# Performance work log

Measured on AMD Instinct MI355X. Metric: run time of the kernel, lower is better.

The kernel has to match this reference:

```python
import jax, jax.numpy as jnp
import numpy as np

N_EMBD = 1024
N_HEAD = 16
HEAD_DIM = N_EMBD // N_HEAD


def setup_inputs() -> dict:
    key = jax.random.key(0)
    ks = jax.random.split(key, 9)
    B, T, C = 2, 2048, N_EMBD
    s = 1.0 / np.sqrt(C)
    inp = {
        "x": jax.random.normal(ks[0], (B, T, C), dtype=jnp.float32),
        "Wq": jax.random.normal(ks[1], (C, C), dtype=jnp.float32) * s,
        "bq": jnp.zeros((C,), dtype=jnp.float32),
        "Wk": jax.random.normal(ks[2], (C, C), dtype=jnp.float32) * s,
        "bk": jnp.zeros((C,), dtype=jnp.float32),
        "Wv": jax.random.normal(ks[3], (C, C), dtype=jnp.float32) * s,
        "bv": jnp.zeros((C,), dtype=jnp.float32),
        "Wo": jax.random.normal(ks[4], (C, C), dtype=jnp.float32) * s,
        "bo": jnp.zeros((C,), dtype=jnp.float32),
    }
    return inp


def reference(x, Wq, bq, Wk, bk, Wv, bv, Wo, bo):
    B, T, C = x.shape
    H, D = N_HEAD, HEAD_DIM
    # projections (torch Linear: x @ W^T + b)
    q = (x @ Wq.T + bq).reshape(B, T, H, D).transpose(0, 2, 1, 3)  # [B,H,T,D]
    k = (x @ Wk.T + bk).reshape(B, T, H, D).transpose(0, 2, 1, 3)
    v = (x @ Wv.T + bv).reshape(B, T, H, D).transpose(0, 2, 1, 3)
    scores = jnp.einsum("bhqd,bhkd->bhqk", q, k) / jnp.sqrt(jnp.asarray(D, x.dtype))
    causal = jnp.tril(jnp.ones((T, T), dtype=bool))
    scores = jnp.where(causal[None, None], scores, jnp.asarray(-jnp.inf, x.dtype))
    weights = jax.nn.softmax(scores, axis=-1)  # [B,H,T,T]
    attended = jnp.einsum("bhqk,bhkd->bhqd", weights, v)
    attended = attended.transpose(0, 2, 1, 3).reshape(B, T, C)
    return attended @ Wo.T + bo
```

## Files before the change

### kernel.cpp

```cpp
#include <hip/hip_runtime.h>

typedef unsigned short u16;
typedef __attribute__((ext_vector_type(8))) __bf16 bf16x8;
typedef __attribute__((ext_vector_type(4))) float f32x4;
typedef __attribute__((ext_vector_type(4))) unsigned int u32x4;

#define MFMA16(a, b, c) __builtin_amdgcn_mfma_f32_16x16x32_bf16(a, b, c, 0, 0, 0)

__device__ __forceinline__ u16 f2bf(float f) {
    unsigned u = __float_as_uint(f);
    u = (u + 0x7FFFu + ((u >> 16) & 1u)) >> 16;
    return (u16)u;
}

__device__ __forceinline__ void gl_lds16(const u16* g, u16* l) {
    __builtin_amdgcn_global_load_lds(
        (const __attribute__((address_space(1))) unsigned int*)g,
        (__attribute__((address_space(3))) unsigned int*)l, 16, 0, 0);
}

static constexpr int Bv = 2, Tv = 2048, Cv = 1024, Hv = 16, Dv = 64;
static constexpr int Mv = Bv * Tv;

static constexpr size_t OFF_XB = 0;
static constexpr size_t OFF_WQ = 4194304;
static constexpr size_t OFF_WK = OFF_WQ + 1048576;
static constexpr size_t OFF_WV = OFF_WK + 1048576;
static constexpr size_t OFF_WO = OFF_WV + 1048576;
static constexpr size_t OFF_Q  = OFF_WO + 1048576;
static constexpr size_t OFF_K  = OFF_Q + 4194304;
static constexpr size_t OFF_V  = OFF_K + 4194304;
static constexpr size_t OFF_A  = OFF_V + 4194304;
static constexpr size_t OFF_VT = OFF_A + 4194304;

__global__ __launch_bounds__(256) void convert_all(
    const float* __restrict__ x,
    const float* __restrict__ wq, const float* __restrict__ wk,
    const float* __restrict__ wv, const float* __restrict__ wo,
    u16* __restrict__ dst)
{
    int i4 = blockIdx.x * blockDim.x + threadIdx.x;
    if (i4 >= 2097152) return;
    int idx = i4 * 4;
    const float* src; int off;
    if (idx < 4194304) { src = x; off = idx; }
    else {
        int rel = idx - 4194304;
        int j = rel >> 20;
        off = rel & 1048575;
        src = (j == 0) ? wq : (j == 1) ? wk : (j == 2) ? wv : wo;
    }
    float4 v = *(const float4*)(src + off);
    ushort4 o;
    o.x = f2bf(v.x); o.y = f2bf(v.y); o.z = f2bf(v.z); o.w = f2bf(v.w);
    *(ushort4*)(dst + idx) = o;
}

template <bool OUT_BF16>
__device__ __forceinline__ void gemm128_body(
    const u16* __restrict__ A, const u16* __restrict__ Wt,
    const float* __restrict__ bias, void* __restrict__ outp,
    int m0, int n0, int N, int K)
{
    __shared__ u16 lA[128 * 32];
    __shared__ u16 lB[128 * 32];
    const int tid  = threadIdx.x;
    const int lane = tid & 63, w = tid >> 6;
    const int quad = lane >> 4, lm = lane & 15;
    const int wm = (w & 1) * 64, wn = (w >> 1) * 64;

    f32x4 zero = {0.f, 0.f, 0.f, 0.f};
    f32x4 acc[4][4];
    #pragma unroll
    for (int mt = 0; mt < 4; mt++)
        #pragma unroll
        for (int nt = 0; nt < 4; nt++) acc[mt][nt] = zero;

    const int srow = lane >> 2, sseg = lane & 3;
    const u16* ga0 = A  + (size_t)(m0 + w * 16 + srow) * K + sseg * 8;
    const u16* ga1 = ga0 + (size_t)64 * K;
    const u16* gb0 = Wt + (size_t)(n0 + w * 16 + srow) * K + sseg * 8;
    const u16* gb1 = gb0 + (size_t)64 * K;
    u16* la0 = &lA[(w * 16) * 32];      u16* la1 = &lA[(64 + w * 16) * 32];
    u16* lb0 = &lB[(w * 16) * 32];      u16* lb1 = &lB[(64 + w * 16) * 32];

    for (int k0 = 0; k0 < K; k0 += 32) {
        gl_lds16(ga0 + k0, la0);
        gl_lds16(ga1 + k0, la1);
        gl_lds16(gb0 + k0, lb0);
        gl_lds16(gb1 + k0, lb1);
        __syncthreads();
        bf16x8 af[4], bf[4];
        #pragma unroll
        for (int mt = 0; mt < 4; mt++)
            af[mt] = *(const bf16x8*)&lA[(wm + mt * 16 + lm) * 32 + quad * 8];
        #pragma unroll
        for (int nt = 0; nt < 4; nt++)
            bf[nt] = *(const bf16x8*)&lB[(wn + nt * 16 + lm) * 32 + quad * 8];
        #pragma unroll
        for (int mt = 0; mt < 4; mt++)
            #pragma unroll
            for (int nt = 0; nt < 4; nt++)
                acc[mt][nt] = MFMA16(af[mt], bf[nt], acc[mt][nt]);
        __syncthreads();
    }

    #pragma unroll
    for (int nt = 0; nt < 4; nt++) {
        int col = n0 + wn + nt * 16 + lm;
        float bv = bias[col];
        #pragma unroll
        for (int mt = 0; mt < 4; mt++) {
            #pragma unroll
            for (int r = 0; r < 4; r++) {
                int row = m0 + wm + mt * 16 + quad * 4 + r;
                float v = acc[mt][nt][r] + bv;
                if (OUT_BF16) ((u16*)outp)[(size_t)row * N + col] = f2bf(v);
                else          ((float*)outp)[(size_t)row * N + col] = v;
            }
        }
    }
}

__global__ __launch_bounds__(256) void gemm_qkv(
    const u16* __restrict__ A,
    const u16* __restrict__ Wq, const u16* __restrict__ Wk, const u16* __restrict__ Wv,
    const float* __restrict__ bq, const float* __restrict__ bk, const float* __restrict__ bv,
    u16* __restrict__ Q, u16* __restrict__ K, u16* __restrict__ V)
{
    int nb = blockIdx.x;
    int which = nb >> 3;
    int n0 = (nb & 7) * 128;
    int m0 = blockIdx.y * 128;
    const u16* Wt = (which == 0) ? Wq : (which == 1) ? Wk : Wv;
    const float* bias = (which == 0) ? bq : (which == 1) ? bk : bv;
    u16* out = (which == 0) ? Q : (which == 1) ? K : V;
    gemm128_body<true>(A, Wt, bias, out, m0, n0, Cv, Cv);
}

__global__ __launch_bounds__(256) void transpose_v(
    const u16* __restrict__ V, u16* __restrict__ VT)
{
    __shared__ u16 t[64][72];
    const int m0 = blockIdx.x * 64, c0 = blockIdx.y * 64;
    const int tid = threadIdx.x;
    const int mr = tid >> 3, cs = tid & 7;
    *(u32x4*)&t[mr][cs * 8]      = *(const u32x4*)(V + (size_t)(m0 + mr) * Cv + c0 + cs * 8);
    *(u32x4*)&t[mr + 32][cs * 8] = *(const u32x4*)(V + (size_t)(m0 + mr + 32) * Cv + c0 + cs * 8);
    __syncthreads();
    const int cr = tid >> 3, ms = tid & 7;
    #pragma unroll
    for (int h2 = 0; h2 < 2; h2++) {
        int c = cr + h2 * 32;
        ushort4 o0, o1;
        o0.x = t[ms * 8 + 0][c]; o0.y = t[ms * 8 + 1][c];
        o0.z = t[ms * 8 + 2][c]; o0.w = t[ms * 8 + 3][c];
        o1.x = t[ms * 8 + 4][c]; o1.y = t[ms * 8 + 5][c];
        o1.z = t[ms * 8 + 6][c]; o1.w = t[ms * 8 + 7][c];
        u16* dst = VT + (size_t)(c0 + c) * Mv + m0 + ms * 8;
        *(ushort4*)(dst)     = o0;
        *(ushort4*)(dst + 4) = o1;
    }
}

__global__ __launch_bounds__(256) void gemm_o64(
    const u16* __restrict__ A, const u16* __restrict__ Wt,
    const float* __restrict__ bias, float* __restrict__ outp)
{
    __shared__ u16 lA[128 * 32];
    __shared__ u16 lB[64 * 32];
    const int tid  = threadIdx.x;
    const int lane = tid & 63, w = tid >> 6;
    const int quad = lane >> 4, lm = lane & 15;
    const int m0 = blockIdx.y * 128, n0 = blockIdx.x * 64;
    const int K = Cv;

    f32x4 zero = {0.f, 0.f, 0.f, 0.f};
    f32x4 acc[2][4];
    #pragma unroll
    for (int mt = 0; mt < 2; mt++)
        #pragma unroll
        for (int nt = 0; nt < 4; nt++) acc[mt][nt] = zero;

    const int srow = lane >> 2, sseg = lane & 3;
    const u16* ga0 = A + (size_t)(m0 + w * 32 + srow) * K + sseg * 8;
    const u16* ga1 = ga0 + (size_t)16 * K;
    const u16* gb  = Wt + (size_t)(n0 + w * 16 + srow) * K + sseg * 8;
    u16* la0 = &lA[(w * 32) * 32];
    u16* la1 = &lA[(w * 32 + 16) * 32];
    u16* lb  = &lB[(w * 16) * 32];

    for (int k0 = 0; k0 < K; k0 += 32) {
        gl_lds16(ga0 + k0, la0);
        gl_lds16(ga1 + k0, la1);
        gl_lds16(gb + k0, lb);
        __syncthreads();
        bf16x8 af[2], bf[4];
        #pragma unroll
        for (int mt = 0; mt < 2; mt++)
            af[mt] = *(const bf16x8*)&lA[(w * 32 + mt * 16 + lm) * 32 + quad * 8];
        #pragma unroll
        for (int nt = 0; nt < 4; nt++)
            bf[nt] = *(const bf16x8*)&lB[(nt * 16 + lm) * 32 + quad * 8];
        #pragma unroll
        for (int mt = 0; mt < 2; mt++)
            #pragma unroll
            for (int nt = 0; nt < 4; nt++)
                acc[mt][nt] = MFMA16(af[mt], bf[nt], acc[mt][nt]);
        __syncthreads();
    }

    #pragma unroll
    for (int nt = 0; nt < 4; nt++) {
        int col = n0 + nt * 16 + lm;
        float bv = bias[col];
        #pragma unroll
        for (int mt = 0; mt < 2; mt++) {
            #pragma unroll
            for (int r = 0; r < 4; r++) {
                int row = m0 + w * 32 + mt * 16 + quad * 4 + r;
                outp[(size_t)row * Cv + col] = acc[mt][nt][r] + bv;
            }
        }
    }
}

__global__ __launch_bounds__(256) void attn(
    const u16* __restrict__ Qp, const u16* __restrict__ Kp,
    const u16* __restrict__ VTg, u16* __restrict__ Op)
{
    __shared__ u16 lK[2][64 * 64];
    __shared__ u16 lVT[2][64 * 64];
    __shared__ u16 lP[4][32][72];

    const int tid  = threadIdx.x;
    const int lane = tid & 63, w = tid >> 6;
    const int quad = lane >> 4, lm = lane & 15;

    const int idx  = blockIdx.x;
    const int half = idx >> 8;
    const int grp  = idx & 255;
    const int bh   = grp >> 3;
    const int j    = grp & 7;
    const int qt   = half ? j : 15 - j;
    const int h = bh & 15, b = bh >> 4;

    const int qb = qt * 128;
    const size_t headoff = (size_t)b * Tv * Cv + (size_t)h * Dv;
    const size_t vthead  = (size_t)h * 64 * Mv + (size_t)b * Tv;

    bf16x8 qf[2][2];
    #pragma unroll
    for (int nt = 0; nt < 2; nt++) {
        const u16* qptr = Qp + headoff + (size_t)(qb + w * 32 + nt * 16 + lm) * Cv + quad * 8;
        qf[0][nt] = *(const bf16x8*)(qptr);
        qf[1][nt] = *(const bf16x8*)(qptr + 32);
    }

    f32x4 zero = {0.f, 0.f, 0.f, 0.f};
    f32x4 oacc[2][4];
    #pragma unroll
    for (int mt = 0; mt < 2; mt++)
        #pragma unroll
        for (int nt = 0; nt < 4; nt++) oacc[mt][nt] = zero;
    float Lp[2] = {0.f, 0.f};

    const float SC = 0.18033688011112042f;
    const int rowi = lane >> 3, seg = lane & 7;
    const int niter = qt * 2 + 2;

    auto stage = [&](int bsel, int kt) {
        const int k0 = kt * 64;
        #pragma unroll
        for (int hf = 0; hf < 2; hf++) {
            int rbase = w * 16 + hf * 8;
            int row = rbase + rowi;
            int gseg = seg ^ (row & 7);
            gl_lds16(Kp + headoff + (size_t)(k0 + row) * Cv + gseg * 8, &lK[bsel][rbase * 64]);
            gl_lds16(VTg + vthead + (size_t)row * Mv + k0 + gseg * 8, &lVT[bsel][rbase * 64]);
        }
    };

    stage(0, 0);

    for (int kt = 0; kt < niter; kt++) {
        const int bsel = kt & 1;
        const int k0 = kt * 64;
        __syncthreads();
        if (kt + 1 < niter) stage(bsel ^ 1, kt + 1);

        f32x4 stt[4][2];
        #pragma unroll
        for (int mt = 0; mt < 4; mt++)
            #pragma unroll
            for (int nt = 0; nt < 2; nt++) stt[mt][nt] = zero;
        #pragma unroll
        for (int ks = 0; ks < 2; ks++) {
            #pragma unroll
            for (int mt = 0; mt < 4; mt++) {
                bf16x8 kf = *(const bf16x8*)
                    &lK[bsel][(mt * 16 + lm) * 64 + (((ks * 4 + quad) ^ (lm & 7)) * 8)];
                #pragma unroll
                for (int nt = 0; nt < 2; nt++)
                    stt[mt][nt] = MFMA16(kf, qf[ks][nt], stt[mt][nt]);
            }
        }

        const bool needmask = (kt >= niter - 2);
        #pragma unroll
        for (int mt = 0; mt < 4; mt++) {
            #pragma unroll
            for (int nt = 0; nt < 2; nt++) {
                const int keyb = k0 + mt * 16 + quad * 4;
                const int qrow = qb + w * 32 + nt * 16 + lm;
                ushort4 pk;
                float e0 = __builtin_amdgcn_exp2f(fmaf(stt[mt][nt][0], SC, -16.f));
                float e1 = __builtin_amdgcn_exp2f(fmaf(stt[mt][nt][1], SC, -16.f));
                float e2 = __builtin_amdgcn_exp2f(fmaf(stt[mt][nt][2], SC, -16.f));
                float e3 = __builtin_amdgcn_exp2f(fmaf(stt[mt][nt][3], SC, -16.f));
                if (needmask) {
                    if (keyb + 0 > qrow) e0 = 0.f;
                    if (keyb + 1 > qrow) e1 = 0.f;
                    if (keyb + 2 > qrow) e2 = 0.f;
                    if (keyb + 3 > qrow) e3 = 0.f;
                }
                Lp[nt] += e0 + e1 + e2 + e3;
                pk.x = (u16)(__float_as_uint(e0) >> 16);
                pk.y = (u16)(__float_as_uint(e1) >> 16);
                pk.z = (u16)(__float_as_uint(e2) >> 16);
                pk.w = (u16)(__float_as_uint(e3) >> 16);
                *(ushort4*)&lP[w][nt * 16 + lm][mt * 16 + quad * 4] = pk;
            }
        }

        #pragma unroll
        for (int ks = 0; ks < 2; ks++) {
            bf16x8 pf[2];
            #pragma unroll
            for (int mt = 0; mt < 2; mt++)
                pf[mt] = *(const bf16x8*)&lP[w][mt * 16 + lm][ks * 32 + quad * 8];
            #pragma unroll
            for (int nt = 0; nt < 4; nt++) {
                bf16x8 vf = *(const bf16x8*)
                    &lVT[bsel][(nt * 16 + lm) * 64 + (((ks * 4 + quad) ^ (lm & 7)) * 8)];
                #pragma unroll
                for (int mt = 0; mt < 2; mt++)
                    oacc[mt][nt] = MFMA16(pf[mt], vf, oacc[mt][nt]);
            }
        }
    }

    float Lred[2];
    #pragma unroll
    for (int nt = 0; nt < 2; nt++) {
        float L = Lp[nt];
        L += __shfl_xor(L, 16, 64);
        L += __shfl_xor(L, 32, 64);
        Lred[nt] = 1.0f / L;
    }
    #pragma unroll
    for (int mt = 0; mt < 2; mt++) {
        float inv[4];
        #pragma unroll
        for (int r = 0; r < 4; r++)
            inv[r] = __shfl(Lred[mt], (lane & 48) | (quad * 4 + r), 64);
        #pragma unroll
        for (int nt = 0; nt < 4; nt++) {
            #pragma unroll
            for (int r = 0; r < 4; r++) {
                int row = qb + w * 32 + mt * 16 + quad * 4 + r;
                Op[headoff + (size_t)row * Cv + nt * 16 + lm] = f2bf(oacc[mt][nt][r] * inv[r]);
            }
        }
    }
}

extern "C" void kernel_launch(void* const* d_in, const int* in_sizes, int n_in,
                              void* d_out, int out_size, void* d_ws, size_t ws_size,
                              hipStream_t stream) {
    const float* x  = (const float*)d_in[0];
    const float* Wq = (const float*)d_in[1];
    const float* bq = (const float*)d_in[2];
    const float* Wk = (const float*)d_in[3];
    const float* bk = (const float*)d_in[4];
    const float* Wv = (const float*)d_in[5];
    const float* bv = (const float*)d_in[6];
    const float* Wo = (const float*)d_in[7];
    const float* bo = (const float*)d_in[8];
    u16* ws = (u16*)d_ws;

    convert_all<<<8192, 256, 0, stream>>>(x, Wq, Wk, Wv, Wo, ws);

    gemm_qkv<<<dim3(24, 32), 256, 0, stream>>>(
        ws + OFF_XB, ws + OFF_WQ, ws + OFF_WK, ws + OFF_WV,
        bq, bk, bv, ws + OFF_Q, ws + OFF_K, ws + OFF_V);

    transpose_v<<<dim3(Mv / 64, Cv / 64), 256, 0, stream>>>(ws + OFF_V, ws + OFF_VT);

    attn<<<512, 256, 0, stream>>>(ws + OFF_Q, ws + OFF_K, ws + OFF_VT, ws + OFF_A);

    gemm_o64<<<dim3(16, 32), 256, 0, stream>>>(ws + OFF_A, ws + OFF_WO, bo, (float*)d_out);
}
```

Baseline: 197.9 us.

## Compute V transposed directly in QKV GEMM and use swizzled 64-wide K tiles

The V projection is computed as Wv·x^T with a row bias, so V^T is written straight from the QKV GEMM and the separate transpose kernel and its extra buffer round trip go away. Both GEMMs also move from 32-wide to 64-wide K tiles with an XOR-swizzled LDS layout, which halves the number of barriers per K and is meant to avoid LDS bank conflicts on the fragment reads. The V^T output is stored with a stride of Mv elements, so those writes may coalesce poorly. The larger tiles double LDS use per block, which could lower occupancy.

```diff
diff --git a/kernel.cpp b/kernel.cpp
--- a/kernel.cpp
+++ b/kernel.cpp
@@ -29,9 +29,8 @@
 static constexpr size_t OFF_WO = OFF_WV + 1048576;
 static constexpr size_t OFF_Q  = OFF_WO + 1048576;
 static constexpr size_t OFF_K  = OFF_Q + 4194304;
-static constexpr size_t OFF_V  = OFF_K + 4194304;
-static constexpr size_t OFF_A  = OFF_V + 4194304;
-static constexpr size_t OFF_VT = OFF_A + 4194304;
+static constexpr size_t OFF_VT = OFF_K + 4194304;
+static constexpr size_t OFF_A  = OFF_VT + 4194304;
 
 __global__ __launch_bounds__(256) void convert_all(
     const float* __restrict__ x,
@@ -56,14 +55,14 @@
     *(ushort4*)(dst + idx) = o;
 }
 
-template <bool OUT_BF16>
-__device__ __forceinline__ void gemm128_body(
+template <bool OUT_BF16, bool ROWBIAS>
+__device__ __forceinline__ void gemm128_b64(
     const u16* __restrict__ A, const u16* __restrict__ Wt,
     const float* __restrict__ bias, void* __restrict__ outp,
     int m0, int n0, int N, int K)
 {
-    __shared__ u16 lA[128 * 32];
-    __shared__ u16 lB[128 * 32];
+    __shared__ u16 lA[128 * 64];
+    __shared__ u16 lB[128 * 64];
     const int tid  = threadIdx.x;
     const int lane = tid & 63, w = tid >> 6;
     const int quad = lane >> 4, lm = lane & 15;
@@ -76,45 +75,47 @@
         #pragma unroll
         for (int nt = 0; nt < 4; nt++) acc[mt][nt] = zero;
 
-    const int srow = lane >> 2, sseg = lane & 3;
-    const u16* ga0 = A  + (size_t)(m0 + w * 16 + srow) * K + sseg * 8;
-    const u16* ga1 = ga0 + (size_t)64 * K;
-    const u16* gb0 = Wt + (size_t)(n0 + w * 16 + srow) * K + sseg * 8;
-    const u16* gb1 = gb0 + (size_t)64 * K;
-    u16* la0 = &lA[(w * 16) * 32];      u16* la1 = &lA[(64 + w * 16) * 32];
-    u16* lb0 = &lB[(w * 16) * 32];      u16* lb1 = &lB[(64 + w * 16) * 32];
-
-    for (int k0 = 0; k0 < K; k0 += 32) {
-        gl_lds16(ga0 + k0, la0);
-        gl_lds16(ga1 + k0, la1);
-        gl_lds16(gb0 + k0, lb0);
-        gl_lds16(gb1 + k0, lb1);
-        __syncthreads();
-        bf16x8 af[4], bf[4];
-        #pragma unroll
-        for (int mt = 0; mt < 4; mt++)
-            af[mt] = *(const bf16x8*)&lA[(wm + mt * 16 + lm) * 32 + quad * 8];
-        #pragma unroll
-        for (int nt = 0; nt < 4; nt++)
-            bf[nt] = *(const bf16x8*)&lB[(wn + nt * 16 + lm) * 32 + quad * 8];
-        #pragma unroll
-        for (int mt = 0; mt < 4; mt++)
+    const int rowi = lane >> 3, seg = lane & 7;
+
+    for (int k0 = 0; k0 < K; k0 += 64) {
+        #pragma unroll
+        for (int i = 0; i < 4; i++) {
+            int rbase = w * 32 + i * 8;
+            int row = rbase + rowi;
+            int gseg = seg ^ (row & 7);
+            gl_lds16(A  + (size_t)(m0 + row) * K + k0 + gseg * 8, &lA[rbase * 64]);
+            gl_lds16(Wt + (size_t)(n0 + row) * K + k0 + gseg * 8, &lB[rbase * 64]);
+        }
+        __syncthreads();
+        #pragma unroll
+        for (int ks = 0; ks < 2; ks++) {
+            const int swz = ((ks * 4 + quad) ^ (lm & 7)) * 8;
+            bf16x8 af[4], bf[4];
+            #pragma unroll
+            for (int mt = 0; mt < 4; mt++)
+                af[mt] = *(const bf16x8*)&lA[(wm + mt * 16 + lm) * 64 + swz];
             #pragma unroll
             for (int nt = 0; nt < 4; nt++)
-                acc[mt][nt] = MFMA16(af[mt], bf[nt], acc[mt][nt]);
+                bf[nt] = *(const bf16x8*)&lB[(wn + nt * 16 + lm) * 64 + swz];
+            #pragma unroll
+            for (int mt = 0; mt < 4; mt++)
+                #pragma unroll
+                for (int nt = 0; nt < 4; nt++)
+                    acc[mt][nt] = MFMA16(af[mt], bf[nt], acc[mt][nt]);
+        }
         __syncthreads();
     }
 
     #pragma unroll
     for (int nt = 0; nt < 4; nt++) {
         int col = n0 + wn + nt * 16 + lm;
-        float bv = bias[col];
+        float cb = ROWBIAS ? 0.f : bias[col];
         #pragma unroll
         for (int mt = 0; mt < 4; mt++) {
             #pragma unroll
             for (int r = 0; r < 4; r++) {
                 int row = m0 + wm + mt * 16 + quad * 4 + r;
-                float v = acc[mt][nt][r] + bv;
+                float v = acc[mt][nt][r] + (ROWBIAS ? bias[row] : cb);
                 if (OUT_BF16) ((u16*)outp)[(size_t)row * N + col] = f2bf(v);
                 else          ((float*)outp)[(size_t)row * N + col] = v;
             }
@@ -126,40 +127,16 @@
     const u16* __restrict__ A,
     const u16* __restrict__ Wq, const u16* __restrict__ Wk, const u16* __restrict__ Wv,
     const float* __restrict__ bq, const float* __restrict__ bk, const float* __restrict__ bv,
-    u16* __restrict__ Q, u16* __restrict__ K, u16* __restrict__ V)
+    u16* __restrict__ Q, u16* __restrict__ K, u16* __restrict__ VT)
 {
     int nb = blockIdx.x;
     int which = nb >> 3;
-    int n0 = (nb & 7) * 128;
-    int m0 = blockIdx.y * 128;
-    const u16* Wt = (which == 0) ? Wq : (which == 1) ? Wk : Wv;
-    const float* bias = (which == 0) ? bq : (which == 1) ? bk : bv;
-    u16* out = (which == 0) ? Q : (which == 1) ? K : V;
-    gemm128_body<true>(A, Wt, bias, out, m0, n0, Cv, Cv);
-}
-
-__global__ __launch_bounds__(256) void transpose_v(
-    const u16* __restrict__ V, u16* __restrict__ VT)
-{
-    __shared__ u16 t[64][72];
-    const int m0 = blockIdx.x * 64, c0 = blockIdx.y * 64;
-    const int tid = threadIdx.x;
-    const int mr = tid >> 3, cs = tid & 7;
-    *(u32x4*)&t[mr][cs * 8]      = *(const u32x4*)(V + (size_t)(m0 + mr) * Cv + c0 + cs * 8);
-    *(u32x4*)&t[mr + 32][cs * 8] = *(const u32x4*)(V + (size_t)(m0 + mr + 32) * Cv + c0 + cs * 8);
-    __syncthreads();
-    const int cr = tid >> 3, ms = tid & 7;
-    #pragma unroll
-    for (int h2 = 0; h2 < 2; h2++) {
-        int c = cr + h2 * 32;
-        ushort4 o0, o1;
-        o0.x = t[ms * 8 + 0][c]; o0.y = t[ms * 8 + 1][c];
-        o0.z = t[ms * 8 + 2][c]; o0.w = t[ms * 8 + 3][c];
-        o1.x = t[ms * 8 + 4][c]; o1.y = t[ms * 8 + 5][c];
-        o1.z = t[ms * 8 + 6][c]; o1.w = t[ms * 8 + 7][c];
-        u16* dst = VT + (size_t)(c0 + c) * Mv + m0 + ms * 8;
-        *(ushort4*)(dst)     = o0;
-        *(ushort4*)(dst + 4) = o1;
+    if (which == 0) {
+        gemm128_b64<true, false>(A, Wq, bq, Q, blockIdx.y * 128, (nb & 7) * 128, Cv, Cv);
+    } else if (which == 1) {
+        gemm128_b64<true, false>(A, Wk, bk, K, blockIdx.y * 128, (nb & 7) * 128, Cv, Cv);
+    } else {
+        gemm128_b64<true, true>(Wv, A, bv, VT, (nb & 7) * 128, blockIdx.y * 128, Mv, Cv);
     }
 }
 
@@ -167,8 +144,8 @@
     const u16* __restrict__ A, const u16* __restrict__ Wt,
     const float* __restrict__ bias, float* __restrict__ outp)
 {
-    __shared__ u16 lA[128 * 32];
-    __shared__ u16 lB[64 * 32];
+    __shared__ u16 lA[128 * 64];
+    __shared__ u16 lB[64 * 64];
     const int tid  = threadIdx.x;
     const int lane = tid & 63, w = tid >> 6;
     const int quad = lane >> 4, lm = lane & 15;
@@ -182,44 +159,51 @@
         #pragma unroll
         for (int nt = 0; nt < 4; nt++) acc[mt][nt] = zero;
 
-    const int srow = lane >> 2, sseg = lane & 3;
-    const u16* ga0 = A + (size_t)(m0 + w * 32 + srow) * K + sseg * 8;
-    const u16* ga1 = ga0 + (size_t)16 * K;
-    const u16* gb  = Wt + (size_t)(n0 + w * 16 + srow) * K + sseg * 8;
-    u16* la0 = &lA[(w * 32) * 32];
-    u16* la1 = &lA[(w * 32 + 16) * 32];
-    u16* lb  = &lB[(w * 16) * 32];
-
-    for (int k0 = 0; k0 < K; k0 += 32) {
-        gl_lds16(ga0 + k0, la0);
-        gl_lds16(ga1 + k0, la1);
-        gl_lds16(gb + k0, lb);
-        __syncthreads();
-        bf16x8 af[2], bf[4];
-        #pragma unroll
-        for (int mt = 0; mt < 2; mt++)
-            af[mt] = *(const bf16x8*)&lA[(w * 32 + mt * 16 + lm) * 32 + quad * 8];
-        #pragma unroll
-        for (int nt = 0; nt < 4; nt++)
-            bf[nt] = *(const bf16x8*)&lB[(nt * 16 + lm) * 32 + quad * 8];
-        #pragma unroll
-        for (int mt = 0; mt < 2; mt++)
+    const int rowi = lane >> 3, seg = lane & 7;
+
+    for (int k0 = 0; k0 < K; k0 += 64) {
+        #pragma unroll
+        for (int i = 0; i < 4; i++) {
+            int rbase = w * 32 + i * 8;
+            int row = rbase + rowi;
+            int gseg = seg ^ (row & 7);
+            gl_lds16(A + (size_t)(m0 + row) * K + k0 + gseg * 8, &lA[rbase * 64]);
+        }
+        {
+            int rbase = w * 16, row0 = rbase + rowi, row1 = row0 + 8;
+            gl_lds16(Wt + (size_t)(n0 + row0) * K + k0 + (seg ^ (row0 & 7)) * 8, &lB[rbase * 64]);
+            gl_lds16(Wt + (size_t)(n0 + row1) * K + k0 + (seg ^ (row1 & 7)) * 8, &lB[(rbase + 8) * 64]);
+        }
+        __syncthreads();
+        #pragma unroll
+        for (int ks = 0; ks < 2; ks++) {
+            const int swz = ((ks * 4 + quad) ^ (lm & 7)) * 8;
+            bf16x8 af[2], bf[4];
+            #pragma unroll
+            for (int mt = 0; mt < 2; mt++)
+                af[mt] = *(const bf16x8*)&lA[(w * 32 + mt * 16 + lm) * 64 + swz];
             #pragma unroll
             for (int nt = 0; nt < 4; nt++)
-                acc[mt][nt] = MFMA16(af[mt], bf[nt], acc[mt][nt]);
+                bf[nt] = *(const bf16x8*)&lB[(nt * 16 + lm) * 64 + swz];
+            #pragma unroll
+            for (int mt = 0; mt < 2; mt++)
+                #pragma unroll
+                for (int nt = 0; nt < 4; nt++)
+                    acc[mt][nt] = MFMA16(af[mt], bf[nt], acc[mt][nt]);
+        }
         __syncthreads();
     }
 
     #pragma unroll
     for (int nt = 0; nt < 4; nt++) {
         int col = n0 + nt * 16 + lm;
-        float bv = bias[col];
+        float bvv = bias[col];
         #pragma unroll
         for (int mt = 0; mt < 2; mt++) {
             #pragma unroll
             for (int r = 0; r < 4; r++) {
                 int row = m0 + w * 32 + mt * 16 + quad * 4 + r;
-                outp[(size_t)row * Cv + col] = acc[mt][nt][r] + bv;
+                outp[(size_t)row * Cv + col] = acc[mt][nt][r] + bvv;
             }
         }
     }
@@ -393,9 +377,7 @@
 
     gemm_qkv<<<dim3(24, 32), 256, 0, stream>>>(
         ws + OFF_XB, ws + OFF_WQ, ws + OFF_WK, ws + OFF_WV,
-        bq, bk, bv, ws + OFF_Q, ws + OFF_K, ws + OFF_V);
-
-    transpose_v<<<dim3(Mv / 64, Cv / 64), 256, 0, stream>>>(ws + OFF_V, ws + OFF_VT);
+        bq, bk, bv, ws + OFF_Q, ws + OFF_K, ws + OFF_VT);
 
     attn<<<512, 256, 0, stream>>>(ws + OFF_Q, ws + OFF_K, ws + OFF_VT, ws + OFF_A);
 
```

Result: no change. 196.4 us (-0.7%).
